# Kernel tuning notes

Hardware: AMD Instinct MI355X
Metric: run time of the kernel (lower is better)

The kernel has to match this reference:

```python
import jax, jax.numpy as jnp
import numpy as np

B, N, NS, D, H = 32, 4096, 16, 512, 8
DH = D // H          # dims_per_head = 64
DFF = 4 * D          # ff_mlp hidden
SCALE = DH ** -0.5
EPS = 1e-8           # slot-attention renorm eps
LN_EPS = 1e-5        # torch LayerNorm default
ITERS = 3


def layer_norm(x, g, b):
    mu = jnp.mean(x, axis=-1, keepdims=True)
    var = jnp.mean((x - mu) ** 2, axis=-1, keepdims=True)
    return (x - mu) * jax.lax.rsqrt(var + LN_EPS) * g + b


def setup_inputs() -> dict:
    key = jax.random.key(0)
    ks = jax.random.split(key, 8)
    s = 0.02
    return {
        "inputs": jax.random.normal(ks[0], (B, N, D), jnp.float32),
        "conditioning": jax.random.normal(ks[1], (B, NS, D), jnp.float32),
        # norm_input
        "ln_in_g": jnp.ones((D,), jnp.float32),
        "ln_in_b": jnp.zeros((D,), jnp.float32),
        # projections (no bias: use_projection_bias=False)
        "Wk": jax.random.normal(ks[2], (D, D), jnp.float32) * s,
        "Wv": jax.random.normal(ks[3], (D, D), jnp.float32) * s,
        "Wq": jax.random.normal(ks[4], (D, D), jnp.float32) * s,
        "Wo": jax.random.normal(ks[5], (D, D), jnp.float32) * s,
        # norm_slots / norm_slots_ff_mlp
        "ln_s_g": jnp.ones((D,), jnp.float32),
        "ln_s_b": jnp.zeros((D,), jnp.float32),
        "ln_f_g": jnp.ones((D,), jnp.float32),
        "ln_f_b": jnp.zeros((D,), jnp.float32),
        # ff_mlp: Linear(D,4D) -> ReLU -> Linear(4D,D)
        "W1": jax.random.normal(ks[6], (D, DFF), jnp.float32) * s,
        "b1": jnp.zeros((DFF,), jnp.float32),
        "W2": jax.random.normal(ks[7], (DFF, D), jnp.float32) * s,
        "b2": jnp.zeros((D,), jnp.float32),
    }


def reference(inputs, conditioning, ln_in_g, ln_in_b, Wk, Wv, Wq, Wo,
              ln_s_g, ln_s_b, ln_f_g, ln_f_b, W1, b1, W2, b2):
    b = inputs.shape[0]
    x = layer_norm(inputs, ln_in_g, ln_in_b)                 # [b, n, D]
    k = (x @ Wk.T).reshape(b, N, H, DH)                      # [b, n, h, dh]
    v = (x @ Wv.T).reshape(b, N, H, DH)

    slots = conditioning
    attn_mean = None
    for _ in range(ITERS):
        slots_prev = slots
        s = layer_norm(slots, ln_s_g, ln_s_b)
        q = (s @ Wq.T).reshape(b, NS, H, DH)                 # [b, ns, h, dh]
        dots = jnp.einsum("bihd,bjhd->bihj", q, k) * SCALE   # [b, ns, h, n]
        # softmax over flattened (slots, heads) axis, per input location j
        attn = jax.nn.softmax(dots.reshape(b, NS * H, N), axis=1)
        attn = attn.reshape(b, NS, H, N)
        attn_before = attn
        attn = attn + EPS
        attn = attn / jnp.sum(attn, axis=-1, keepdims=True)  # renorm over j
        updates = jnp.einsum("bjhd,bihj->bihd", v, attn)     # [b, ns, h, dh]
        updates = updates.reshape(b, NS, D)
        slots = updates @ Wo.T + slots_prev                  # to_o + residual
        slots_prev_ff = slots
        s2 = layer_norm(slots, ln_f_g, ln_f_b)
        s2 = jax.nn.relu(s2 @ W1 + b1) @ W2 + b2             # ff_mlp
        slots = s2 + slots_prev_ff
        attn_mean = jnp.mean(attn_before, axis=2)            # [b, ns, n]
    return slots, attn_mean
```

## Files before the change

### kernel.cpp

```cpp
#include <hip/hip_runtime.h>
#include <cstdint>
#include <cstddef>

typedef __attribute__((ext_vector_type(8))) short short8;
typedef __attribute__((ext_vector_type(4))) short short4v;
typedef __attribute__((ext_vector_type(8))) __bf16 bf16x8;
typedef __attribute__((ext_vector_type(4))) float f32x4;
typedef unsigned short u16;

static constexpr int Bb = 32, Nn = 4096, NSs = 16, Dd = 512, Hh = 8, DFF = 2048;
static constexpr float SCALE = 0.125f;
static constexpr float EPSR  = 1e-8f;
static constexpr float LN_EPS = 1e-5f;

__device__ __forceinline__ u16 f2b(float x) {
  union { float f; uint32_t u; } a; a.f = x;
  uint32_t r = a.u + 0x7fffu + ((a.u >> 16) & 1u);
  return (u16)(r >> 16);
}

__device__ __forceinline__ f32x4 mfma16(short8 a, short8 b, f32x4 c) {
  return __builtin_amdgcn_mfma_f32_16x16x32_bf16(
      __builtin_bit_cast(bf16x8, a), __builtin_bit_cast(bf16x8, b), c, 0, 0, 0);
}

__device__ __forceinline__ void gload16(const u16* g, u16* l) {
  __builtin_amdgcn_global_load_lds(
      (const __attribute__((address_space(1))) void*)g,
      (__attribute__((address_space(3))) void*)l, 16, 0, 0);
}

__global__ __launch_bounds__(256) void ln_rows(const float* __restrict__ src,
    const float* __restrict__ g, const float* __restrict__ bt,
    u16* __restrict__ dst, int R) {
  int row = blockIdx.x * 4 + (threadIdx.x >> 6);
  if (row >= R) return;
  int lane = threadIdx.x & 63;
  const float* p = src + (size_t)row * Dd + lane * 8;
  float4 u0 = *(const float4*)p;
  float4 u1 = *(const float4*)(p + 4);
  float x[8] = {u0.x,u0.y,u0.z,u0.w,u1.x,u1.y,u1.z,u1.w};
  float s = 0.f, s2 = 0.f;
#pragma unroll
  for (int e = 0; e < 8; ++e) { s += x[e]; s2 += x[e]*x[e]; }
#pragma unroll
  for (int m = 1; m < 64; m <<= 1) { s += __shfl_xor(s, m); s2 += __shfl_xor(s2, m); }
  float mean = s * (1.f/512.f);
  float var  = s2 * (1.f/512.f) - mean*mean;
  float rstd = rsqrtf(var + LN_EPS);
  union { u16 o[8]; short8 v; } ou;
#pragma unroll
  for (int e = 0; e < 8; ++e)
    ou.o[e] = f2b((x[e]-mean)*rstd*g[lane*8+e] + bt[lane*8+e]);
  *(short8*)(dst + (size_t)row * Dd + lane * 8) = ou.v;
}

__global__ __launch_bounds__(256, 2) void gemm_kv(const u16* __restrict__ A,
    const u16* __restrict__ Bk, const u16* __restrict__ Bv,
    u16* __restrict__ Ck, u16* __restrict__ CvT) {
  __shared__ u16 lA[128*64];
  __shared__ u16 lK[128*64];
  __shared__ u16 lV[128*64];
  const int tid = threadIdx.x, lane = tid & 63, wid = tid >> 6;
  const int wr = wid >> 1, wc = wid & 1;
  const int n  = blockIdx.y * 4 + blockIdx.x;
  const int orig = (n & 7) * 512 + (n >> 3);
  const int bm = (orig >> 2) * 128, bn = (orig & 3) * 128;
  const size_t BN = (size_t)Bb * Nn;
  f32x4 ak[4][4] = {};
  f32x4 av[4][4] = {};
  const int sr = lane >> 3;
  const int ss = ((lane & 7) ^ (sr & 7)) * 8;
  const int li = lane & 15, lk = lane >> 4;
  const int sx = (li & 7) * 8;
  for (int t = 0; t < 8; ++t) {
    const int k0 = t * 64;
    __syncthreads();
#pragma unroll
    for (int gi = 0; gi < 4; ++gi) {
      const int rb = wid * 32 + gi * 8;
      gload16(A  + (size_t)(bm + rb + sr) * Dd + k0 + ss, &lA[rb * 64]);
      gload16(Bk + (size_t)(bn + rb + sr) * Dd + k0 + ss, &lK[rb * 64]);
      gload16(Bv + (size_t)(bn + rb + sr) * Dd + k0 + ss, &lV[rb * 64]);
    }
    __syncthreads();
#pragma unroll
    for (int kk = 0; kk < 2; ++kk) {
      const int cs = ((kk * 4 + lk) * 8) ^ sx;
      short8 af[4], kf[4], vf[4];
#pragma unroll
      for (int m = 0; m < 4; ++m)
        af[m] = *(const short8*)&lA[(wr*64 + m*16 + li)*64 + cs];
#pragma unroll
      for (int nn2 = 0; nn2 < 4; ++nn2) {
        kf[nn2] = *(const short8*)&lK[(wc*64 + nn2*16 + li)*64 + cs];
        vf[nn2] = *(const short8*)&lV[(wc*64 + nn2*16 + li)*64 + cs];
      }
#pragma unroll
      for (int m = 0; m < 4; ++m)
#pragma unroll
        for (int nn2 = 0; nn2 < 4; ++nn2) {
          ak[m][nn2] = mfma16(af[m], kf[nn2], ak[m][nn2]);
          av[m][nn2] = mfma16(af[m], vf[nn2], av[m][nn2]);
        }
    }
  }
  const int lr = lk * 4;
#pragma unroll
  for (int m = 0; m < 4; ++m)
#pragma unroll
    for (int nn2 = 0; nn2 < 4; ++nn2) {
      int row = bm + wr*64 + m*16 + lr;
      int col = bn + wc*64 + nn2*16 + li;
      f32x4 vk = ak[m][nn2];
#pragma unroll
      for (int r = 0; r < 4; ++r)
        Ck[(size_t)(row + r) * Dd + col] = f2b(vk[r]);
      f32x4 vv = av[m][nn2];
      union { u16 o[4]; short4v v4; } ou;
#pragma unroll
      for (int r = 0; r < 4; ++r) ou.o[r] = f2b(vv[r]);
      *(short4v*)&CvT[(size_t)col * BN + row] = ou.v4;
    }
}

template<int EP>
__global__ __launch_bounds__(256) void gemm64(const u16* __restrict__ A,
    const u16* __restrict__ Bw, void* __restrict__ Cp,
    const float* __restrict__ bias, const float* __restrict__ res,
    int N, int K) {
  const int lane = threadIdx.x & 63, wid = threadIdx.x >> 6;
  const int wr = wid >> 1, wc = wid & 1;
  const int bm = blockIdx.y * 64, bn = blockIdx.x * 64;
  const int li = lane & 15, lk = lane >> 4;
  f32x4 acc[2][2] = {};
  const u16* Ap = A  + (size_t)(bm + wr*32 + li) * K + lk*8;
  const u16* Bp = Bw + (size_t)(bn + wc*32 + li) * K + lk*8;
#pragma unroll 4
  for (int k0 = 0; k0 < K; k0 += 32) {
    short8 af[2], bf[2];
    af[0] = *(const short8*)(Ap + k0);
    af[1] = *(const short8*)(Ap + (size_t)16*K + k0);
    bf[0] = *(const short8*)(Bp + k0);
    bf[1] = *(const short8*)(Bp + (size_t)16*K + k0);
#pragma unroll
    for (int m = 0; m < 2; ++m)
#pragma unroll
      for (int nn2 = 0; nn2 < 2; ++nn2)
        acc[m][nn2] = mfma16(af[m], bf[nn2], acc[m][nn2]);
  }
  const int lr = lk * 4;
#pragma unroll
  for (int m = 0; m < 2; ++m)
#pragma unroll
    for (int nn2 = 0; nn2 < 2; ++nn2) {
      int row = bm + wr*32 + m*16 + lr;
      int col = bn + wc*32 + nn2*16 + li;
      f32x4 v = acc[m][nn2];
#pragma unroll
      for (int r = 0; r < 4; ++r) {
        size_t off = (size_t)(row + r) * N + col;
        float x = v[r];
        if constexpr (EP == 0) ((u16*)Cp)[off] = f2b(x);
        else if constexpr (EP == 1) ((float*)Cp)[off] = x + res[off];
        else if constexpr (EP == 2) { x += bias[col]; ((u16*)Cp)[off] = f2b(x > 0.f ? x : 0.f); }
        else ((float*)Cp)[off] = x + bias[col] + res[off];
      }
    }
}

__global__ __launch_bounds__(512) void attn_f(const u16* __restrict__ q,
    const u16* __restrict__ kk, const u16* __restrict__ vT,
    float* __restrict__ rowsum, float* __restrict__ Tpart,
    float* __restrict__ attn_mean) {
  const int js = blockIdx.x, b = blockIdx.y;
  const int tid = threadIdx.x, lane = tid & 63;
  const int h = tid >> 6;
  __shared__ float sc[64][129];
  __shared__ float red[8][64];
  __shared__ u16 P2[8][16][72];
  const int li = lane & 15, lk = lane >> 4;
  const size_t BN = (size_t)Bb * Nn;
  const u16* qb = q + (((size_t)b*16 + li)*8 + h)*64 + lk*8;
  short8 a0 = *(const short8*)qb;
  short8 a1 = *(const short8*)(qb + 32);
  f32x4 apv[4] = {};
  float rs_acc = 0.f;
  const int jl = tid & 63, qt = tid >> 6;
  for (int t2 = 0; t2 < 8; ++t2) {
    const int j0 = js * 512 + t2 * 64;
#pragma unroll
    for (int n = 0; n < 4; ++n) {
      const u16* kb = kk + ((size_t)b*Nn + j0 + n*16 + li)*Dd + h*64 + lk*8;
      f32x4 acc = {};
      acc = mfma16(a0, *(const short8*)kb, acc);
      acc = mfma16(a1, *(const short8*)(kb + 32), acc);
#pragma unroll
      for (int r = 0; r < 4; ++r)
        sc[n*16 + li][(lk*4 + r)*8 + h] = acc[r] * SCALE;
    }
    __syncthreads();
    float mx = -1e30f;
#pragma unroll
    for (int e = 0; e < 16; ++e) mx = fmaxf(mx, sc[jl][qt*16 + e]);
    red[qt][jl] = mx;
    __syncthreads();
    float M = red[0][jl];
#pragma unroll
    for (int p = 1; p < 8; ++p) M = fmaxf(M, red[p][jl]);
    __syncthreads();
    float s = 0.f;
#pragma unroll
    for (int e = 0; e < 16; ++e) {
      float ev = __expf(sc[jl][qt*16 + e] - M);
      sc[jl][qt*16 + e] = ev; s += ev;
    }
    red[qt][jl] = s;
    __syncthreads();
    float S = red[0][jl];
#pragma unroll
    for (int p = 1; p < 8; ++p) S += red[p][jl];
    float inv = 1.f / S;
#pragma unroll
    for (int e = 0; e < 16; ++e) {
      int ih = qt*16 + e;
      float a = sc[jl][ih] * inv + EPSR;
      sc[jl][ih] = a;
      P2[ih & 7][ih >> 3][jl] = f2b(a);
    }
    __syncthreads();
    if (tid < 128) {
      float rs = 0.f;
      for (int j2 = 0; j2 < 64; ++j2) rs += sc[j2][tid];
      rs_acc += rs;
    }
    if (attn_mean != nullptr && tid < 64) {
      for (int i = 0; i < 16; ++i) {
        float sm = 0.f;
#pragma unroll
        for (int hh = 0; hh < 8; ++hh) sm += sc[tid][i*8 + hh];
        attn_mean[((size_t)b*16 + i)*Nn + j0 + tid] = sm * 0.125f - EPSR;
      }
    }
#pragma unroll
    for (int n = 0; n < 4; ++n) {
      const u16* vb = vT + (size_t)(h*64 + n*16 + li)*BN + (size_t)b*Nn + j0 + lk*8;
      short8 b0 = *(const short8*)vb;
      short8 b1 = *(const short8*)(vb + 32);
      short8 pa0 = *(const short8*)&P2[h][li][lk*8];
      short8 pa1 = *(const short8*)&P2[h][li][32 + lk*8];
      apv[n] = mfma16(pa0, b0, apv[n]);
      apv[n] = mfma16(pa1, b1, apv[n]);
    }
    __syncthreads();
  }
  float* Tout = Tpart + (((size_t)js * Bb + b) * 8 + h) * 16 * 64;
#pragma unroll
  for (int n = 0; n < 4; ++n)
#pragma unroll
    for (int r = 0; r < 4; ++r)
      Tout[(size_t)(lk*4 + r) * 64 + n*16 + li] = apv[n][r];
  if (tid < 128) atomicAdd(&rowsum[b*128 + tid], rs_acc);
}

__global__ void upd_c(const float* __restrict__ Tpart,
    const float* __restrict__ rs, u16* __restrict__ updb) {
  int idx = blockIdx.x * 256 + threadIdx.x;
  int o = idx & 511, bi = idx >> 9;
  int b = bi >> 4, i = bi & 15;
  int h = o >> 6, d = o & 63;
  size_t base = (((size_t)b * 8 + h) * 16 + i) * 64 + d;
  const size_t stride = (size_t)Bb * 8 * 16 * 64;
  float t = 0.f;
#pragma unroll
  for (int p = 0; p < 8; ++p) t += Tpart[base + p * stride];
  updb[idx] = f2b(t / rs[b * 128 + i * 8 + h]);
}

__global__ void cvt_w(const float* __restrict__ s, u16* __restrict__ d, int n) {
  int i = blockIdx.x*256 + threadIdx.x;
  if (i < n) d[i] = f2b(s[i]);
}
__global__ __launch_bounds__(256) void tr_cvt(const float* __restrict__ s,
    u16* __restrict__ d, int R, int C) {
  __shared__ u16 t[32][33];
  const int c0 = blockIdx.x*32, r0 = blockIdx.y*32;
  const int tr = threadIdx.x >> 3, tc4 = (threadIdx.x & 7)*4;
  float4 v = *(const float4*)&s[(size_t)(r0+tr)*C + c0 + tc4];
  t[tr][tc4+0] = f2b(v.x); t[tr][tc4+1] = f2b(v.y);
  t[tr][tc4+2] = f2b(v.z); t[tr][tc4+3] = f2b(v.w);
  __syncthreads();
  const int oc = threadIdx.x >> 3, or4 = (threadIdx.x & 7)*4;
  union { u16 o[4]; short4v v4; } ou;
#pragma unroll
  for (int e = 0; e < 4; ++e) ou.o[e] = t[or4+e][oc];
  *(short4v*)&d[(size_t)(c0+oc)*R + r0 + or4] = ou.v4;
}
__global__ void copy_f32v4(const float* __restrict__ s, float* __restrict__ d, int n4) {
  int i = blockIdx.x*256 + threadIdx.x;
  if (i < n4) ((float4*)d)[i] = ((const float4*)s)[i];
}

extern "C" void kernel_launch(void* const* d_in, const int* in_sizes, int n_in,
                              void* d_out, int out_size, void* d_ws, size_t ws_size,
                              hipStream_t stream) {
  (void)in_sizes; (void)n_in; (void)out_size; (void)ws_size;
  const float* inputs  = (const float*)d_in[0];
  const float* cond    = (const float*)d_in[1];
  const float* ln_in_g = (const float*)d_in[2];
  const float* ln_in_b = (const float*)d_in[3];
  const float* Wk = (const float*)d_in[4];
  const float* Wv = (const float*)d_in[5];
  const float* Wq = (const float*)d_in[6];
  const float* Wo = (const float*)d_in[7];
  const float* ln_s_g = (const float*)d_in[8];
  const float* ln_s_b = (const float*)d_in[9];
  const float* ln_f_g = (const float*)d_in[10];
  const float* ln_f_b = (const float*)d_in[11];
  const float* W1 = (const float*)d_in[12];
  const float* b1 = (const float*)d_in[13];
  const float* W2 = (const float*)d_in[14];
  const float* b2 = (const float*)d_in[15];
  float* out_slots = (float*)d_out;
  float* out_amean = (float*)d_out + (size_t)Bb*NSs*Dd;

  char* w = (char*)d_ws;
  auto alloc = [&](size_t bytes) {
    char* p = w; w += (bytes + 255) & ~(size_t)255; return p;
  };
  u16*  xn    = (u16*)alloc((size_t)Bb*Nn*Dd*2);
  u16*  kbuf  = (u16*)alloc((size_t)Bb*Nn*Dd*2);
  u16*  vT    = (u16*)alloc((size_t)Bb*Nn*Dd*2);
  float* Tpart = (float*)alloc((size_t)8*Bb*8*16*64*4);
  float* slots = (float*)alloc((size_t)Bb*NSs*Dd*4);
  u16*  qb    = (u16*)alloc((size_t)Bb*NSs*Dd*2);
  u16*  snb   = (u16*)alloc((size_t)Bb*NSs*Dd*2);
  u16*  s2nb  = (u16*)alloc((size_t)Bb*NSs*Dd*2);
  u16*  h1b   = (u16*)alloc((size_t)Bb*NSs*DFF*2);
  u16*  updb  = (u16*)alloc((size_t)Bb*NSs*Dd*2);
  float* rowsum = (float*)alloc((size_t)Bb*128*3*4);
  u16*  wkb = (u16*)alloc(262144*2);
  u16*  wvb = (u16*)alloc(262144*2);
  u16*  wqb = (u16*)alloc(262144*2);
  u16*  wob = (u16*)alloc(262144*2);
  u16*  w1t = (u16*)alloc((size_t)1048576*2);
  u16*  w2t = (u16*)alloc((size_t)1048576*2);

  cvt_w<<<1024, 256, 0, stream>>>(Wk, wkb, 262144);
  cvt_w<<<1024, 256, 0, stream>>>(Wv, wvb, 262144);
  cvt_w<<<1024, 256, 0, stream>>>(Wq, wqb, 262144);
  cvt_w<<<1024, 256, 0, stream>>>(Wo, wob, 262144);
  tr_cvt<<<dim3(64, 16), 256, 0, stream>>>(W1, w1t, 512, 2048);
  tr_cvt<<<dim3(16, 64), 256, 0, stream>>>(W2, w2t, 2048, 512);
  copy_f32v4<<<256, 256, 0, stream>>>(cond, slots, 65536);
  (void)hipMemsetAsync(rowsum, 0, (size_t)Bb*128*3*4, stream);
  ln_rows<<<Bb*Nn/4, 256, 0, stream>>>(inputs, ln_in_g, ln_in_b, xn, Bb*Nn);
  gemm_kv<<<dim3(4, Bb*Nn/128), 256, 0, stream>>>(xn, wkb, wvb, kbuf, vT);

  for (int it = 0; it < 3; ++it) {
    float* rsp = rowsum + (size_t)it * Bb * 128;
    ln_rows<<<128, 256, 0, stream>>>(slots, ln_s_g, ln_s_b, snb, Bb*NSs);
    gemm64<0><<<dim3(8, 8), 256, 0, stream>>>(snb, wqb, qb, nullptr, nullptr, 512, 512);
    attn_f<<<dim3(8, Bb), 512, 0, stream>>>(qb, kbuf, vT, rsp, Tpart,
                                            it == 2 ? out_amean : nullptr);
    upd_c<<<1024, 256, 0, stream>>>(Tpart, rsp, updb);
    gemm64<1><<<dim3(8, 8), 256, 0, stream>>>(updb, wob, slots, nullptr, slots, 512, 512);
    ln_rows<<<128, 256, 0, stream>>>(slots, ln_f_g, ln_f_b, s2nb, Bb*NSs);
    gemm64<2><<<dim3(32, 8), 256, 0, stream>>>(s2nb, w1t, h1b, b1, nullptr, 2048, 512);
    gemm64<3><<<dim3(8, 8), 256, 0, stream>>>(h1b, w2t, slots, b2, slots, 512, 2048);
  }
  copy_f32v4<<<256, 256, 0, stream>>>(slots, out_slots, 65536);
}
```

Baseline: 730.2 us.

## Keep softmax scores in registers and split sequence across more attention blocks

Rewrites the attention kernel so the scaled dot products stay in MFMA accumulator registers. The cross-head softmax max/sum are reduced with lane shuffles plus a small shared buffer, replacing the large shared score tile and several barriers. The sequence split per batch is doubled so more blocks run concurrently, and a launch-bounds occupancy hint is added. attn_mean is now computed from the bf16 probabilities, which adds a small amount of rounding, and the update reduction must sum twice as many partials.

```diff
diff --git a/kernel.cpp b/kernel.cpp
--- a/kernel.cpp
+++ b/kernel.cpp
@@ -12,11 +12,15 @@
 static constexpr float SCALE = 0.125f;
 static constexpr float EPSR  = 1e-8f;
 static constexpr float LN_EPS = 1e-5f;
+static constexpr int JS = 16;
 
 __device__ __forceinline__ u16 f2b(float x) {
   union { float f; uint32_t u; } a; a.f = x;
   uint32_t r = a.u + 0x7fffu + ((a.u >> 16) & 1u);
   return (u16)(r >> 16);
+}
+__device__ __forceinline__ float b2f(u16 x) {
+  union { uint32_t u; float f; } a; a.u = ((uint32_t)x) << 16; return a.f;
 }
 
 __device__ __forceinline__ f32x4 mfma16(short8 a, short8 b, f32x4 c) {
@@ -169,15 +173,14 @@
     }
 }
 
-__global__ __launch_bounds__(512) void attn_f(const u16* __restrict__ q,
+__global__ __launch_bounds__(512, 4) void attn_f(const u16* __restrict__ q,
     const u16* __restrict__ kk, const u16* __restrict__ vT,
     float* __restrict__ rowsum, float* __restrict__ Tpart,
     float* __restrict__ attn_mean) {
   const int js = blockIdx.x, b = blockIdx.y;
-  const int tid = threadIdx.x, lane = tid & 63;
-  const int h = tid >> 6;
-  __shared__ float sc[64][129];
-  __shared__ float red[8][64];
+  const int tid = threadIdx.x, lane = tid & 63, h = tid >> 6;
+  __shared__ float redM[8][64];
+  __shared__ float redS[8][64];
   __shared__ u16 P2[8][16][72];
   const int li = lane & 15, lk = lane >> 4;
   const size_t BN = (size_t)Bb * Nn;
@@ -185,10 +188,10 @@
   short8 a0 = *(const short8*)qb;
   short8 a1 = *(const short8*)(qb + 32);
   f32x4 apv[4] = {};
-  float rs_acc = 0.f;
-  const int jl = tid & 63, qt = tid >> 6;
-  for (int t2 = 0; t2 < 8; ++t2) {
-    const int j0 = js * 512 + t2 * 64;
+  float rs_acc[4] = {0.f, 0.f, 0.f, 0.f};
+  for (int t2 = 0; t2 < 4; ++t2) {
+    const int j0 = js * 256 + t2 * 64;
+    f32x4 dt[4];
 #pragma unroll
     for (int n = 0; n < 4; ++n) {
       const u16* kb = kk + ((size_t)b*Nn + j0 + n*16 + li)*Dd + h*64 + lk*8;
@@ -196,63 +199,76 @@
       acc = mfma16(a0, *(const short8*)kb, acc);
       acc = mfma16(a1, *(const short8*)(kb + 32), acc);
 #pragma unroll
+      for (int r = 0; r < 4; ++r) dt[n][r] = acc[r] * SCALE;
+    }
+#pragma unroll
+    for (int n = 0; n < 4; ++n) {
+      float v = fmaxf(fmaxf(dt[n][0], dt[n][1]), fmaxf(dt[n][2], dt[n][3]));
+      v = fmaxf(v, __shfl_xor(v, 16));
+      v = fmaxf(v, __shfl_xor(v, 32));
+      if (lk == 0) redM[h][n*16 + li] = v;
+    }
+    __syncthreads();
+    float M[4];
+#pragma unroll
+    for (int n = 0; n < 4; ++n) {
+      float m2 = redM[0][n*16 + li];
+#pragma unroll
+      for (int p = 1; p < 8; ++p) m2 = fmaxf(m2, redM[p][n*16 + li]);
+      M[n] = m2;
+    }
+#pragma unroll
+    for (int n = 0; n < 4; ++n) {
+      float s = 0.f;
+#pragma unroll
+      for (int r = 0; r < 4; ++r) { dt[n][r] = __expf(dt[n][r] - M[n]); s += dt[n][r]; }
+      s += __shfl_xor(s, 16);
+      s += __shfl_xor(s, 32);
+      if (lk == 0) redS[h][n*16 + li] = s;
+    }
+    __syncthreads();
+#pragma unroll
+    for (int n = 0; n < 4; ++n) {
+      float s2 = redS[0][n*16 + li];
+#pragma unroll
+      for (int p = 1; p < 8; ++p) s2 += redS[p][n*16 + li];
+      float inv = 1.f / s2;
+#pragma unroll
+      for (int r = 0; r < 4; ++r) dt[n][r] = dt[n][r] * inv + EPSR;
+    }
+#pragma unroll
+    for (int n = 0; n < 4; ++n)
+#pragma unroll
       for (int r = 0; r < 4; ++r)
-        sc[n*16 + li][(lk*4 + r)*8 + h] = acc[r] * SCALE;
-    }
-    __syncthreads();
-    float mx = -1e30f;
-#pragma unroll
-    for (int e = 0; e < 16; ++e) mx = fmaxf(mx, sc[jl][qt*16 + e]);
-    red[qt][jl] = mx;
-    __syncthreads();
-    float M = red[0][jl];
-#pragma unroll
-    for (int p = 1; p < 8; ++p) M = fmaxf(M, red[p][jl]);
-    __syncthreads();
-    float s = 0.f;
-#pragma unroll
-    for (int e = 0; e < 16; ++e) {
-      float ev = __expf(sc[jl][qt*16 + e] - M);
-      sc[jl][qt*16 + e] = ev; s += ev;
-    }
-    red[qt][jl] = s;
-    __syncthreads();
-    float S = red[0][jl];
-#pragma unroll
-    for (int p = 1; p < 8; ++p) S += red[p][jl];
-    float inv = 1.f / S;
-#pragma unroll
-    for (int e = 0; e < 16; ++e) {
-      int ih = qt*16 + e;
-      float a = sc[jl][ih] * inv + EPSR;
-      sc[jl][ih] = a;
-      P2[ih & 7][ih >> 3][jl] = f2b(a);
-    }
-    __syncthreads();
-    if (tid < 128) {
-      float rs = 0.f;
-      for (int j2 = 0; j2 < 64; ++j2) rs += sc[j2][tid];
-      rs_acc += rs;
-    }
-    if (attn_mean != nullptr && tid < 64) {
-      for (int i = 0; i < 16; ++i) {
+        P2[h][lk*4 + r][n*16 + li] = f2b(dt[n][r]);
+#pragma unroll
+    for (int r = 0; r < 4; ++r) {
+      float v = dt[0][r] + dt[1][r] + dt[2][r] + dt[3][r];
+      v += __shfl_xor(v, 1); v += __shfl_xor(v, 2);
+      v += __shfl_xor(v, 4); v += __shfl_xor(v, 8);
+      rs_acc[r] += v;
+    }
+    short8 pa0 = *(const short8*)&P2[h][li][lk*8];
+    short8 pa1 = *(const short8*)&P2[h][li][32 + lk*8];
+#pragma unroll
+    for (int n = 0; n < 4; ++n) {
+      const u16* vb = vT + (size_t)(h*64 + n*16 + li)*BN + (size_t)b*Nn + j0 + lk*8;
+      apv[n] = mfma16(pa0, *(const short8*)vb, apv[n]);
+      apv[n] = mfma16(pa1, *(const short8*)(vb + 32), apv[n]);
+    }
+    if (attn_mean != nullptr) {
+      __syncthreads();
+      int j = tid & 63;
+#pragma unroll
+      for (int ii = 0; ii < 2; ++ii) {
+        int i = (tid >> 6) + ii*8;
         float sm = 0.f;
 #pragma unroll
-        for (int hh = 0; hh < 8; ++hh) sm += sc[tid][i*8 + hh];
-        attn_mean[((size_t)b*16 + i)*Nn + j0 + tid] = sm * 0.125f - EPSR;
+        for (int hh = 0; hh < 8; ++hh) sm += b2f(P2[hh][i][j]);
+        attn_mean[((size_t)b*16 + i)*Nn + j0 + j] = sm * 0.125f - EPSR;
       }
-    }
-#pragma unroll
-    for (int n = 0; n < 4; ++n) {
-      const u16* vb = vT + (size_t)(h*64 + n*16 + li)*BN + (size_t)b*Nn + j0 + lk*8;
-      short8 b0 = *(const short8*)vb;
-      short8 b1 = *(const short8*)(vb + 32);
-      short8 pa0 = *(const short8*)&P2[h][li][lk*8];
-      short8 pa1 = *(const short8*)&P2[h][li][32 + lk*8];
-      apv[n] = mfma16(pa0, b0, apv[n]);
-      apv[n] = mfma16(pa1, b1, apv[n]);
-    }
-    __syncthreads();
+      __syncthreads();
+    }
   }
   float* Tout = Tpart + (((size_t)js * Bb + b) * 8 + h) * 16 * 64;
 #pragma unroll
@@ -260,7 +276,10 @@
 #pragma unroll
     for (int r = 0; r < 4; ++r)
       Tout[(size_t)(lk*4 + r) * 64 + n*16 + li] = apv[n][r];
-  if (tid < 128) atomicAdd(&rowsum[b*128 + tid], rs_acc);
+  if (li == 0)
+#pragma unroll
+    for (int r = 0; r < 4; ++r)
+      atomicAdd(&rowsum[b*128 + (lk*4 + r)*8 + h], rs_acc[r]);
 }
 
 __global__ void upd_c(const float* __restrict__ Tpart,
@@ -273,7 +292,7 @@
   const size_t stride = (size_t)Bb * 8 * 16 * 64;
   float t = 0.f;
 #pragma unroll
-  for (int p = 0; p < 8; ++p) t += Tpart[base + p * stride];
+  for (int p = 0; p < JS; ++p) t += Tpart[base + p * stride];
   updb[idx] = f2b(t / rs[b * 128 + i * 8 + h]);
 }
 
@@ -331,7 +350,7 @@
   u16*  xn    = (u16*)alloc((size_t)Bb*Nn*Dd*2);
   u16*  kbuf  = (u16*)alloc((size_t)Bb*Nn*Dd*2);
   u16*  vT    = (u16*)alloc((size_t)Bb*Nn*Dd*2);
-  float* Tpart = (float*)alloc((size_t)8*Bb*8*16*64*4);
+  float* Tpart = (float*)alloc((size_t)JS*Bb*8*16*64*4);
   float* slots = (float*)alloc((size_t)Bb*NSs*Dd*4);
   u16*  qb    = (u16*)alloc((size_t)Bb*NSs*Dd*2);
   u16*  snb   = (u16*)alloc((size_t)Bb*NSs*Dd*2);
@@ -361,8 +380,8 @@
     float* rsp = rowsum + (size_t)it * Bb * 128;
     ln_rows<<<128, 256, 0, stream>>>(slots, ln_s_g, ln_s_b, snb, Bb*NSs);
     gemm64<0><<<dim3(8, 8), 256, 0, stream>>>(snb, wqb, qb, nullptr, nullptr, 512, 512);
-    attn_f<<<dim3(8, Bb), 512, 0, stream>>>(qb, kbuf, vT, rsp, Tpart,
-                                            it == 2 ? out_amean : nullptr);
+    attn_f<<<dim3(JS, Bb), 512, 0, stream>>>(qb, kbuf, vT, rsp, Tpart,
+                                             it == 2 ? out_amean : nullptr);
     upd_c<<<1024, 256, 0, stream>>>(Tpart, rsp, updb);
     gemm64<1><<<dim3(8, 8), 256, 0, stream>>>(updb, wob, slots, nullptr, slots, 512, 512);
     ln_rows<<<128, 256, 0, stream>>>(slots, ln_f_g, ln_f_b, s2nb, Bb*NSs);
```

Result: faster. 702.0 us (-3.9%).
